# Kernel tuning notes

Hardware: AMD Instinct MI355X
Metric: run time of the kernel (lower is better)

## Reference

```python
import jax, jax.numpy as jnp
import numpy as np

EMB_DIM = 1024
H = 16
HEAD_DIM = EMB_DIM // H
B = 2
S = 2048  # enc and dec seq len
LN_EPS = 1e-5


def setup_inputs() -> dict:
    key = jax.random.key(0)
    ks = jax.random.split(key, 8)
    scale_in = 1.0 / np.sqrt(EMB_DIM)
    scale_o = 1.0 / np.sqrt(H * HEAD_DIM)
    return {
        "enc_out": jax.random.normal(ks[0], (B, S, EMB_DIM), jnp.float32),
        "dec_out": jax.random.normal(ks[1], (B, S, EMB_DIM), jnp.float32),
        # stacked per-head projections, equivalent to h separate Linear(emb_dim, head_dim, bias=False)
        "Wq": jax.random.uniform(ks[2], (H, EMB_DIM, HEAD_DIM), jnp.float32, -scale_in, scale_in),
        "Wk": jax.random.uniform(ks[3], (H, EMB_DIM, HEAD_DIM), jnp.float32, -scale_in, scale_in),
        "Wv": jax.random.uniform(ks[4], (H, EMB_DIM, HEAD_DIM), jnp.float32, -scale_in, scale_in),
        "Wo": jax.random.uniform(ks[5], (H * HEAD_DIM, EMB_DIM), jnp.float32, -scale_o, scale_o),
        "gamma": jnp.ones((EMB_DIM,), jnp.float32),
        "beta": jnp.zeros((EMB_DIM,), jnp.float32),
    }


def reference(enc_out, dec_out, Wq, Wk, Wv, Wo, gamma, beta):
    d = Wq.shape[-1]
    # per-head projections, batched over heads (same math as the Python loop)
    q = jnp.einsum('bse,hed->bhsd', dec_out, Wq)   # queries from decoder
    k = jnp.einsum('bte,hed->bhtd', enc_out, Wk)   # keys from encoder
    v = jnp.einsum('bte,hed->bhtd', enc_out, Wv)   # values from encoder
    scores = jnp.einsum('bhsd,bhtd->bhst', q, k) / jnp.sqrt(jnp.asarray(d, q.dtype))
    att = jax.nn.softmax(scores, axis=-1)
    ctx = jnp.einsum('bhst,bhtd->bhsd', att, v)
    b, h, s, hd = ctx.shape
    ctx = ctx.transpose(0, 2, 1, 3).reshape(b, s, h * hd)  # concat heads along feature dim
    transformed = ctx @ Wo  # dropout is identity in eval mode
    x = dec_out + transformed
    mu = jnp.mean(x, axis=-1, keepdims=True)
    var = jnp.mean(jnp.square(x - mu), axis=-1, keepdims=True)
    return (x - mu) * jax.lax.rsqrt(var + LN_EPS) * gamma + beta
```

## Files before the change

### kernel.cpp

```cpp
#include <hip/hip_runtime.h>
#include <hip/hip_bf16.h>

#define EMB   1024
#define NH    16
#define HD    64
#define SEQ   2048
#define SA    72

typedef __attribute__((ext_vector_type(8))) short          bf16x8;
typedef __attribute__((ext_vector_type(8))) unsigned short us8;
typedef __attribute__((ext_vector_type(4))) float          f32x4;

__device__ __forceinline__ float u2f(unsigned short u) {
    return __uint_as_float(((unsigned)u) << 16);
}
__device__ __forceinline__ unsigned short f2u(float f) {
    __hip_bfloat16 b = __float2bfloat16(f);
    return *reinterpret_cast<unsigned short*>(&b);
}
__device__ __forceinline__ bool detect_bf16(const void* gamma) {
    return ((const unsigned short*)gamma)[0] == 0x3F80;
}
__device__ __forceinline__ f32x4 fzero() {
    f32x4 v; v.x = v.y = v.z = v.w = 0.f; return v;
}
__device__ __forceinline__ void ld16f(const void* p, size_t idx, bool isbf, float* o) {
    if (isbf) {
        const unsigned short* b = (const unsigned short*)p + idx;
        us8 v0 = *(const us8*)b, v1 = *(const us8*)(b + 8);
        #pragma unroll
        for (int i = 0; i < 8; ++i) { o[i] = u2f(v0[i]); o[8 + i] = u2f(v1[i]); }
    } else {
        const float* f = (const float*)p + idx;
        #pragma unroll
        for (int i = 0; i < 4; ++i) {
            float4 v = *(const float4*)(f + 4 * i);
            o[4*i] = v.x; o[4*i+1] = v.y; o[4*i+2] = v.z; o[4*i+3] = v.w;
        }
    }
}
__device__ __forceinline__ float ld1f(const void* p, size_t i, bool isbf) {
    return isbf ? u2f(((const unsigned short*)p)[i]) : ((const float*)p)[i];
}
__device__ __forceinline__ float4 ld4(const void* p, size_t idx, bool isbf) {
    if (isbf) {
        ushort4 t = *reinterpret_cast<const ushort4*>((const unsigned short*)p + idx);
        return make_float4(u2f(t.x), u2f(t.y), u2f(t.z), u2f(t.w));
    }
    return *reinterpret_cast<const float4*>((const float*)p + idx);
}
__device__ __forceinline__ us8 pk8(const float* s) {
    us8 v;
    #pragma unroll
    for (int i = 0; i < 8; ++i) v[i] = f2u(s[i]);
    return v;
}
__device__ __forceinline__ f32x4 mfma16(bf16x8 a, bf16x8 b, f32x4 c) {
    return __builtin_amdgcn_mfma_f32_16x16x32_bf16(a, b, c, 0, 0, 0);
}
__device__ __forceinline__ bf16x8 mk8(unsigned w0, unsigned w1, unsigned w2, unsigned w3) {
    union { unsigned u[4]; bf16x8 v; } x;
    x.u[0] = w0; x.u[1] = w1; x.u[2] = w2; x.u[3] = w3;
    return x.v;
}
__device__ __forceinline__ float fexp2(float x) {
    return __builtin_amdgcn_exp2f(x);
}
__device__ __forceinline__ unsigned cvtpk(float lo, float hi) {
    unsigned r;
    asm("v_cvt_pk_bf16_f32 %0, %1, %2" : "=v"(r) : "v"(lo), "v"(hi));
    return r;
}
__device__ __forceinline__ void gl_lds16(const unsigned short* g, unsigned short* l) {
    __builtin_amdgcn_global_load_lds(
        (const __attribute__((address_space(1))) void*)g,
        (__attribute__((address_space(3))) void*)l,
        16, 0, 0);
}

#define QSCALE 0.18033688f

__global__ __launch_bounds__(256) void prep_kernel(
    const void* __restrict__ dec, const void* __restrict__ enc,
    const void* __restrict__ Wq, const void* __restrict__ Wk,
    const void* __restrict__ Wv, const void* __restrict__ Wo,
    const void* __restrict__ gamma,
    unsigned short* __restrict__ xb,
    unsigned short* __restrict__ wt,
    unsigned short* __restrict__ wot)
{
    const bool isbf = detect_bf16(gamma);
    const int blk = blockIdx.x;
    __shared__ unsigned short T[64][SA];

    if (blk < 2048) {
        const size_t HALF = (size_t)4096 * 1024;
        size_t idx = ((size_t)blk * 256 + threadIdx.x) * 16;
        const void* src; size_t off;
        if (idx < HALF) { src = dec; off = idx; } else { src = enc; off = idx - HALF; }
        float buf[16];
        ld16f(src, off, isbf, buf);
        *(us8*)&xb[idx]     = pk8(buf);
        *(us8*)&xb[idx + 8] = pk8(buf + 8);
    } else if (blk < 2816) {
        const int local = blk - 2048;
        const int which = local >> 8, h = (local >> 4) & 15, e0 = (local & 15) * 64;
        const void* W = (which == 0) ? Wq : (which == 1 ? Wk : Wv);
        const int sr = threadIdx.x >> 2, sc = (threadIdx.x & 3) * 16;

        float buf[16];
        ld16f(W, ((size_t)h * EMB + e0 + sr) * HD + sc, isbf, buf);
        #pragma unroll
        for (int i = 0; i < 16; ++i) T[sc + i][sr] = f2u(buf[i]);
        __syncthreads();
        us8 v0 = *(const us8*)&T[sr][sc];
        us8 v1 = *(const us8*)&T[sr][sc + 8];
        size_t o = (((size_t)which * NH + h) * HD + sr) * EMB + e0 + sc;
        *(us8*)&wt[o] = v0;
        *(us8*)&wt[o + 8] = v1;
    } else {
        const int local = blk - 2816;
        const int n0 = (local & 15) * 64, k0 = (local >> 4) * 64;
        const int sr = threadIdx.x >> 2, sc = (threadIdx.x & 3) * 16;

        float buf[16];
        ld16f(Wo, (size_t)(k0 + sr) * EMB + n0 + sc, isbf, buf);
        #pragma unroll
        for (int i = 0; i < 16; ++i) T[sc + i][sr] = f2u(buf[i]);
        __syncthreads();
        us8 v0 = *(const us8*)&T[sr][sc];
        us8 v1 = *(const us8*)&T[sr][sc + 8];
        size_t o = (size_t)(n0 + sr) * EMB + k0 + sc;
        *(us8*)&wot[o] = v0;
        *(us8*)&wot[o + 8] = v1;
    }
}

__global__ __launch_bounds__(256) void qkv_kernel(
    const unsigned short* __restrict__ xb,
    const unsigned short* __restrict__ wt,
    unsigned short* __restrict__ qo, unsigned short* __restrict__ ko,
    unsigned short* __restrict__ vt)
{
    const int id = blockIdx.x;
    const int xcd = id & 7, sl = id >> 3;
    const int m_t = xcd * 4 + (sl & 3);
    const int n_t = sl >> 2;
    const int m0 = m_t * 128, n0g = n_t * 128;
    const int which = n0g >> 10;
    const int nloc = n0g & 1023;
    const unsigned short* X = xb + ((which == 0) ? (size_t)0 : (size_t)4096 * 1024);

    __shared__ unsigned short smem[17408];
    unsigned short* const ldsA = smem;
    unsigned short* const ldsB = smem + 8192;

    const int tid = threadIdx.x, wv = tid >> 6, lane = tid & 63;
    const int lq = lane >> 4, lm = lane & 15;
    const int mw = (wv & 1) * 64, nw = (wv >> 1) * 64;

    const unsigned short* Wb = wt + (size_t)(which * 1024 + nloc) * EMB;

    const int seg0 = wv * 4;
    const int srow = lane >> 3;
    const int su   = (lane & 7) ^ srow;
    const unsigned short* aP[4];
    const unsigned short* bP[4];
    #pragma unroll
    for (int q = 0; q < 4; ++q) {
        const int s = seg0 + q;
        aP[q] = X  + (size_t)(m0 + 8 * s + srow) * EMB + su * 8;
        bP[q] = Wb + (size_t)(8 * s + srow) * EMB + su * 8;
    }

    f32x4 acc[4][4];
    #pragma unroll
    for (int i = 0; i < 4; ++i)
        #pragma unroll
        for (int j = 0; j < 4; ++j) acc[i][j] = fzero();

    const int xa = lm & 7;

    for (int k0 = 0; k0 < EMB; k0 += 64) {
        #pragma unroll
        for (int q = 0; q < 4; ++q) {
            gl_lds16(aP[q] + k0, ldsA + (seg0 + q) * 512);
            gl_lds16(bP[q] + k0, ldsB + (seg0 + q) * 512);
        }
        asm volatile("s_waitcnt vmcnt(0)" ::: "memory");
        __syncthreads();

        #pragma unroll
        for (int st = 0; st < 2; ++st) {
            const int u = (st * 4 + lq) ^ xa;
            bf16x8 af[4], bq[4];
            #pragma unroll
            for (int i = 0; i < 4; ++i)
                af[i] = *(const bf16x8*)(ldsA + (mw + i * 16 + lm) * 64 + u * 8);
            #pragma unroll
            for (int j = 0; j < 4; ++j)
                bq[j] = *(const bf16x8*)(ldsB + (nw + j * 16 + lm) * 64 + u * 8);
            #pragma unroll
            for (int i = 0; i < 4; ++i)
                #pragma unroll
                for (int j = 0; j < 4; ++j)
                    acc[i][j] = mfma16(af[i], bq[j], acc[i][j]);
        }
        __syncthreads();
    }

    const int b = m0 >> 11, s0 = m0 & (SEQ - 1);
    const float osc = (which == 0) ? QSCALE : 1.0f;
    if (which != 2) {
        unsigned short* Y = which ? ko : qo;
        #pragma unroll
        for (int i = 0; i < 4; ++i)
            #pragma unroll
            for (int j = 0; j < 4; ++j)
                #pragma unroll
                for (int r = 0; r < 4; ++r) {
                    int m = mw + i * 16 + lq * 4 + r;
                    int n = nloc + nw + j * 16 + lm;
                    int h = n >> 6, d = n & 63;
                    Y[(((size_t)b * NH + h) * SEQ + s0 + m) * HD + d] = f2u(acc[i][j][r] * osc);
                }
    } else {
        __syncthreads();
        unsigned short* vbuf = smem;
        #pragma unroll
        for (int i = 0; i < 4; ++i)
            #pragma unroll
            for (int j = 0; j < 4; ++j) {
                ushort4 p;
                p.x = f2u(acc[i][j][0]); p.y = f2u(acc[i][j][1]);
                p.z = f2u(acc[i][j][2]); p.w = f2u(acc[i][j][3]);
                *(ushort4*)&vbuf[(size_t)(nw + j * 16 + lm) * 136 + mw + i * 16 + lq * 4] = p;
            }
        __syncthreads();
        const int dd = tid >> 1, cc = (tid & 1) * 64;
        const int n = nloc + dd, h = n >> 6, d = n & 63;
        size_t o = (((size_t)b * NH + h) * HD + d) * SEQ + s0 + cc;
        #pragma unroll
        for (int jj = 0; jj < 8; ++jj)
            *(us8*)&vt[o + 8 * jj] = *(const us8*)&vbuf[(size_t)dd * 136 + cc + 8 * jj];
    }
}

__global__ __launch_bounds__(128) void attn_kernel(
    const unsigned short* __restrict__ qg,
    const unsigned short* __restrict__ kg,
    const unsigned short* __restrict__ vtg,
    unsigned short* __restrict__ ctx)
{
    __shared__ unsigned short Ks[2][4096];
    __shared__ unsigned short Vt[2][4096];

    const int tid = threadIdx.x, wv = tid >> 6, lane = tid & 63;
    const int lq = lane >> 4, lm = lane & 15;
    const int bh = blockIdx.x, q0 = blockIdx.y * 64;
    const unsigned short* Kg = kg + (size_t)bh * SEQ * HD;
    const unsigned short* Vg = vtg + (size_t)bh * HD * SEQ;

    const int srow = lane >> 3;
    const int su   = (lane & 7) ^ srow;
    const unsigned short* kSp[4];
    const unsigned short* vSp[4];
    #pragma unroll
    for (int j = 0; j < 4; ++j) {
        const int seg = wv + 2 * j;
        kSp[j] = Kg + (size_t)(8 * seg + srow) * HD  + su * 8;
        vSp[j] = Vg + (size_t)(8 * seg + srow) * SEQ + su * 8;
    }

    bf16x8 qf[2][2];
    #pragma unroll
    for (int s = 0; s < 2; ++s)
        #pragma unroll
        for (int st = 0; st < 2; ++st)
            qf[s][st] = *(const bf16x8*)(qg + (size_t)bh * SEQ * HD
                          + (size_t)(q0 + wv * 32 + s * 16 + lm) * HD + st * 32 + lq * 8);

    bf16x8 onesf;
    #pragma unroll
    for (int i = 0; i < 8; ++i) onesf[i] = (short)0x3F80;

    f32x4 Of[2][4], lacc[2];
    #pragma unroll
    for (int s = 0; s < 2; ++s) {
        lacc[s] = fzero();
        #pragma unroll
        for (int t = 0; t < 4; ++t) Of[s][t] = fzero();
    }

    const int xa = lm & 7;

    #pragma unroll
    for (int j = 0; j < 4; ++j) {
        gl_lds16(kSp[j], &Ks[0][(wv + 2 * j) * 512]);
        gl_lds16(vSp[j], &Vt[0][(wv + 2 * j) * 512]);
    }

    for (int it = 0; it < SEQ / 64; ++it) {
        const int cur = it & 1;
        if (it + 1 < SEQ / 64) {
            const size_t ko = (size_t)(it + 1) * 64 * HD;
            const int    vo = (it + 1) * 64;
            #pragma unroll
            for (int j = 0; j < 4; ++j) {
                gl_lds16(kSp[j] + ko, &Ks[cur ^ 1][(wv + 2 * j) * 512]);
                gl_lds16(vSp[j] + vo, &Vt[cur ^ 1][(wv + 2 * j) * 512]);
            }
            asm volatile("s_waitcnt vmcnt(8)" ::: "memory");
        } else {
            asm volatile("s_waitcnt vmcnt(0)" ::: "memory");
        }
        __syncthreads();

        f32x4 sf[2][4];
        #pragma unroll
        for (int s = 0; s < 2; ++s)
            #pragma unroll
            for (int t = 0; t < 4; ++t) sf[s][t] = fzero();
        __builtin_amdgcn_s_setprio(1);
        #pragma unroll
        for (int st = 0; st < 2; ++st) {
            const int u = (st * 4 + lq) ^ xa;
            #pragma unroll
            for (int tt = 0; tt < 4; ++tt) {
                bf16x8 kf = *(const bf16x8*)&Ks[cur][(lm + 16 * tt) * 64 + u * 8];
                sf[0][tt] = mfma16(kf, qf[0][st], sf[0][tt]);
                sf[1][tt] = mfma16(kf, qf[1][st], sf[1][tt]);
            }
        }
        __builtin_amdgcn_s_setprio(0);

        unsigned pw[2][4][2];
        #pragma unroll
        for (int s = 0; s < 2; ++s)
            #pragma unroll
            for (int tt = 0; tt < 4; ++tt) {
                pw[s][tt][0] = cvtpk(fexp2(sf[s][tt][0]), fexp2(sf[s][tt][1]));
                pw[s][tt][1] = cvtpk(fexp2(sf[s][tt][2]), fexp2(sf[s][tt][3]));
            }
        #pragma unroll
        for (int s = 0; s < 2; ++s)
            #pragma unroll
            for (int a = 0; a < 2; ++a)
                #pragma unroll
                for (int c = 0; c < 2; ++c)
                    asm("v_permlane32_swap_b32 %0, %1"
                        : "+v"(pw[s][2 * a][c]), "+v"(pw[s][2 * a + 1][c]));
        #pragma unroll
        for (int s = 0; s < 2; ++s)
            #pragma unroll
            for (int a = 0; a < 2; ++a)
                #pragma unroll
                for (int c = 0; c < 2; ++c)
                    asm("v_permlane16_swap_b32 %0, %1"
                        : "+v"(pw[s][2 * a][c]), "+v"(pw[s][2 * a + 1][c]));

        __builtin_amdgcn_s_setprio(1);
        #pragma unroll
        for (int st = 0; st < 2; ++st) {
            const int u = (st * 4 + lq) ^ xa;
            bf16x8 pf0 = mk8(pw[0][2 * st][0], pw[0][2 * st][1],
                             pw[0][2 * st + 1][0], pw[0][2 * st + 1][1]);
            bf16x8 pf1 = mk8(pw[1][2 * st][0], pw[1][2 * st][1],
                             pw[1][2 * st + 1][0], pw[1][2 * st + 1][1]);
            #pragma unroll
            for (int t = 0; t < 4; ++t) {
                bf16x8 vf = *(const bf16x8*)&Vt[cur][(lm + 16 * t) * 64 + u * 8];
                Of[0][t] = mfma16(pf0, vf, Of[0][t]);
                Of[1][t] = mfma16(pf1, vf, Of[1][t]);
            }
            lacc[0] = mfma16(pf0, onesf, lacc[0]);
            lacc[1] = mfma16(pf1, onesf, lacc[1]);
        }
        __builtin_amdgcn_s_setprio(0);
        __syncthreads();
    }

    const int b = bh >> 4, h = bh & 15;
    #pragma unroll
    for (int s = 0; s < 2; ++s)
        #pragma unroll
        for (int r = 0; r < 4; ++r) {
            float inv = 1.0f / lacc[s][r];
            int srow2 = q0 + wv * 32 + s * 16 + lq * 4 + r;
            #pragma unroll
            for (int t = 0; t < 4; ++t) {
                int d = lm + 16 * t;
                ctx[((size_t)b * SEQ + srow2) * EMB + h * HD + d] = f2u(Of[s][t][r] * inv);
            }
        }
}

__global__ __launch_bounds__(256) void oproj_kernel(
    const unsigned short* __restrict__ ctx,
    const unsigned short* __restrict__ wot,
    const void* __restrict__ dec, const void* __restrict__ gamma,
    float* __restrict__ x)
{
    const bool isbf = detect_bf16(gamma);
    const int id = blockIdx.x;
    const int xcd = id & 7, sl = id >> 3;
    const int m0 = (xcd * 4 + (sl & 3)) * 128;
    const int n0 = (sl >> 2) * 128;

    __shared__ unsigned short smem[16384];
    unsigned short* const ldsA = smem;
    unsigned short* const ldsB = smem + 8192;

    const int tid = threadIdx.x, wv = tid >> 6, lane = tid & 63;
    const int lq = lane >> 4, lm = lane & 15;
    const int mw = (wv & 1) * 64, nw = (wv >> 1) * 64;

    const int seg0 = wv * 4;
    const int srow = lane >> 3;
    const int su   = (lane & 7) ^ srow;
    const unsigned short* aP[4];
    const unsigned short* bP[4];
    #pragma unroll
    for (int q = 0; q < 4; ++q) {
        const int s = seg0 + q;
        aP[q] = ctx + (size_t)(m0 + 8 * s + srow) * EMB + su * 8;
        bP[q] = wot + (size_t)(n0 + 8 * s + srow) * EMB + su * 8;
    }

    f32x4 acc[4][4];
    #pragma unroll
    for (int i = 0; i < 4; ++i)
        #pragma unroll
        for (int j = 0; j < 4; ++j) acc[i][j] = fzero();

    const int xa = lm & 7;

    for (int k0 = 0; k0 < EMB; k0 += 64) {
        #pragma unroll
        for (int q = 0; q < 4; ++q) {
            gl_lds16(aP[q] + k0, ldsA + (seg0 + q) * 512);
            gl_lds16(bP[q] + k0, ldsB + (seg0 + q) * 512);
        }
        asm volatile("s_waitcnt vmcnt(0)" ::: "memory");
        __syncthreads();

        #pragma unroll
        for (int st = 0; st < 2; ++st) {
            const int u = (st * 4 + lq) ^ xa;
            bf16x8 af[4], bq[4];
            #pragma unroll
            for (int i = 0; i < 4; ++i)
                af[i] = *(const bf16x8*)(ldsA + (mw + i * 16 + lm) * 64 + u * 8);
            #pragma unroll
            for (int j = 0; j < 4; ++j)
                bq[j] = *(const bf16x8*)(ldsB + (nw + j * 16 + lm) * 64 + u * 8);
            #pragma unroll
            for (int i = 0; i < 4; ++i)
                #pragma unroll
                for (int j = 0; j < 4; ++j)
                    acc[i][j] = mfma16(af[i], bq[j], acc[i][j]);
        }
        __syncthreads();
    }

    #pragma unroll
    for (int i = 0; i < 4; ++i)
        #pragma unroll
        for (int j = 0; j < 4; ++j)
            #pragma unroll
            for (int r = 0; r < 4; ++r) {
                int m = m0 + mw + i * 16 + lq * 4 + r;
                int n = n0 + nw + j * 16 + lm;
                x[(size_t)m * EMB + n] = acc[i][j][r] + ld1f(dec, (size_t)m * EMB + n, isbf);
            }
}

__global__ __launch_bounds__(256) void ln_kernel(
    const float* __restrict__ x,
    const void* __restrict__ gamma,
    const void* __restrict__ beta,
    void* __restrict__ out)
{
    const bool isbf = detect_bf16(gamma);
    const int row = blockIdx.x;
    const int tid = threadIdx.x;
    const float* xr = x + (size_t)row * EMB;

    float4 xv = *reinterpret_cast<const float4*>(&xr[tid * 4]);
    float s1 = xv.x + xv.y + xv.z + xv.w;
    float s2 = xv.x * xv.x + xv.y * xv.y + xv.z * xv.z + xv.w * xv.w;

    #pragma unroll
    for (int off = 32; off > 0; off >>= 1) {
        s1 += __shfl_down(s1, off);
        s2 += __shfl_down(s2, off);
    }
    __shared__ float w1[4], w2[4];
    const int wid = tid >> 6, lane = tid & 63;
    if (lane == 0) { w1[wid] = s1; w2[wid] = s2; }
    __syncthreads();
    s1 = w1[0] + w1[1] + w1[2] + w1[3];
    s2 = w2[0] + w2[1] + w2[2] + w2[3];

    const float mu  = s1 * (1.0f / EMB);
    const float var = s2 * (1.0f / EMB) - mu * mu;
    const float rs  = rsqrtf(var + 1e-5f);

    float4 gv = ld4(gamma, (size_t)tid * 4, isbf);
    float4 bv = ld4(beta,  (size_t)tid * 4, isbf);
    float4 r;
    r.x = (xv.x - mu) * rs * gv.x + bv.x;
    r.y = (xv.y - mu) * rs * gv.y + bv.y;
    r.z = (xv.z - mu) * rs * gv.z + bv.z;
    r.w = (xv.w - mu) * rs * gv.w + bv.w;

    size_t o = (size_t)row * EMB + tid * 4;
    if (isbf) {
        ushort4 w;
        w.x = f2u(r.x); w.y = f2u(r.y); w.z = f2u(r.z); w.w = f2u(r.w);
        *reinterpret_cast<ushort4*>((unsigned short*)out + o) = w;
    } else {
        *reinterpret_cast<float4*>((float*)out + o) = r;
    }
}

extern "C" void kernel_launch(void* const* d_in, const int* in_sizes, int n_in,
                              void* d_out, int out_size, void* d_ws, size_t ws_size,
                              hipStream_t stream)
{
    const void* enc   = d_in[0];
    const void* dec   = d_in[1];
    const void* Wq    = d_in[2];
    const void* Wk    = d_in[3];
    const void* Wv    = d_in[4];
    const void* Wo    = d_in[5];
    const void* gamma = d_in[6];
    const void* beta  = d_in[7];

    char* w = (char*)d_ws;
    unsigned short* qws  = (unsigned short*)(w);
    unsigned short* kws  = (unsigned short*)(w + (size_t)8  * 1024 * 1024);
    unsigned short* vtws = (unsigned short*)(w + (size_t)16 * 1024 * 1024);
    unsigned short* wtws = (unsigned short*)(w + (size_t)24 * 1024 * 1024);
    unsigned short* wotw = (unsigned short*)(w + (size_t)30 * 1024 * 1024);
    float*          xws  = (float*)         (w);
    unsigned short* xbuf = (unsigned short*)d_out;
    unsigned short* cws  = (unsigned short*)d_out;

    prep_kernel  <<<3072,          256, 0, stream>>>(dec, enc, Wq, Wk, Wv, Wo,
                                                     gamma, xbuf, wtws, wotw);
    qkv_kernel   <<<768,           256, 0, stream>>>(xbuf, wtws, qws, kws, vtws);
    attn_kernel  <<<dim3(32, 32),  128, 0, stream>>>(qws, kws, vtws, cws);
    oproj_kernel <<<256,           256, 0, stream>>>(cws, wotw, dec, gamma, xws);
    ln_kernel    <<<4096,          256, 0, stream>>>(xws, gamma, beta, d_out);
}
```

Before: 239.5 us.

## Split attention KV tile across wave pairs and reduce partial outputs in LDS

The attention block grows from 2 to 4 waves. Each pair of waves handles the same 32 query rows but a different half of each 64-key tile, so per-wave score, exp and PV work is halved. The partial O and row-sum accumulators are combined through shared memory before the final normalization and store. This adds parallelism and latency hiding per block, at the cost of more threads per block, an extra LDS reduction and barrier at the end, and per-wave loads of the full V tile.

```diff
diff --git a/kernel.cpp b/kernel.cpp
--- a/kernel.cpp
+++ b/kernel.cpp
@@ -246,28 +246,29 @@
     }
 }
 
-__global__ __launch_bounds__(128) void attn_kernel(
+__global__ __launch_bounds__(256) void attn_kernel(
     const unsigned short* __restrict__ qg,
     const unsigned short* __restrict__ kg,
     const unsigned short* __restrict__ vtg,
     unsigned short* __restrict__ ctx)
 {
-    __shared__ unsigned short Ks[2][4096];
-    __shared__ unsigned short Vt[2][4096];
+    __shared__ unsigned short smem[16384];
 
     const int tid = threadIdx.x, wv = tid >> 6, lane = tid & 63;
     const int lq = lane >> 4, lm = lane & 15;
+    const int qh  = wv & 1;
+    const int kvh = wv >> 1;
     const int bh = blockIdx.x, q0 = blockIdx.y * 64;
     const unsigned short* Kg = kg + (size_t)bh * SEQ * HD;
     const unsigned short* Vg = vtg + (size_t)bh * HD * SEQ;
 
     const int srow = lane >> 3;
     const int su   = (lane & 7) ^ srow;
-    const unsigned short* kSp[4];
-    const unsigned short* vSp[4];
-    #pragma unroll
-    for (int j = 0; j < 4; ++j) {
-        const int seg = wv + 2 * j;
+    const unsigned short* kSp[2];
+    const unsigned short* vSp[2];
+    #pragma unroll
+    for (int j = 0; j < 2; ++j) {
+        const int seg = wv + 4 * j;
         kSp[j] = Kg + (size_t)(8 * seg + srow) * HD  + su * 8;
         vSp[j] = Vg + (size_t)(8 * seg + srow) * SEQ + su * 8;
     }
@@ -278,7 +279,7 @@
         #pragma unroll
         for (int st = 0; st < 2; ++st)
             qf[s][st] = *(const bf16x8*)(qg + (size_t)bh * SEQ * HD
-                          + (size_t)(q0 + wv * 32 + s * 16 + lm) * HD + st * 32 + lq * 8);
+                          + (size_t)(q0 + qh * 32 + s * 16 + lm) * HD + st * 32 + lq * 8);
 
     bf16x8 onesf;
     #pragma unroll
@@ -293,83 +294,81 @@
     }
 
     const int xa = lm & 7;
-
-    #pragma unroll
-    for (int j = 0; j < 4; ++j) {
-        gl_lds16(kSp[j], &Ks[0][(wv + 2 * j) * 512]);
-        gl_lds16(vSp[j], &Vt[0][(wv + 2 * j) * 512]);
+    const int uv = (kvh * 4 + lq) ^ xa;
+
+    #pragma unroll
+    for (int j = 0; j < 2; ++j) {
+        gl_lds16(kSp[j], smem + (wv + 4 * j) * 512);
+        gl_lds16(vSp[j], smem + 8192 + (wv + 4 * j) * 512);
     }
 
     for (int it = 0; it < SEQ / 64; ++it) {
         const int cur = it & 1;
+        unsigned short* const Kc = smem + cur * 4096;
+        unsigned short* const Vc = smem + 8192 + cur * 4096;
         if (it + 1 < SEQ / 64) {
             const size_t ko = (size_t)(it + 1) * 64 * HD;
             const int    vo = (it + 1) * 64;
-            #pragma unroll
-            for (int j = 0; j < 4; ++j) {
-                gl_lds16(kSp[j] + ko, &Ks[cur ^ 1][(wv + 2 * j) * 512]);
-                gl_lds16(vSp[j] + vo, &Vt[cur ^ 1][(wv + 2 * j) * 512]);
-            }
-            asm volatile("s_waitcnt vmcnt(8)" ::: "memory");
+            unsigned short* const Kn = smem + (cur ^ 1) * 4096;
+            unsigned short* const Vn = smem + 8192 + (cur ^ 1) * 4096;
+            #pragma unroll
+            for (int j = 0; j < 2; ++j) {
+                gl_lds16(kSp[j] + ko, Kn + (wv + 4 * j) * 512);
+                gl_lds16(vSp[j] + vo, Vn + (wv + 4 * j) * 512);
+            }
+            asm volatile("s_waitcnt vmcnt(4)" ::: "memory");
         } else {
             asm volatile("s_waitcnt vmcnt(0)" ::: "memory");
         }
         __syncthreads();
 
-        f32x4 sf[2][4];
+        f32x4 sf[2][2];
         #pragma unroll
         for (int s = 0; s < 2; ++s)
             #pragma unroll
-            for (int t = 0; t < 4; ++t) sf[s][t] = fzero();
+            for (int t = 0; t < 2; ++t) sf[s][t] = fzero();
         __builtin_amdgcn_s_setprio(1);
         #pragma unroll
         for (int st = 0; st < 2; ++st) {
             const int u = (st * 4 + lq) ^ xa;
             #pragma unroll
-            for (int tt = 0; tt < 4; ++tt) {
-                bf16x8 kf = *(const bf16x8*)&Ks[cur][(lm + 16 * tt) * 64 + u * 8];
+            for (int tt = 0; tt < 2; ++tt) {
+                const int ttg = 2 * kvh + tt;
+                bf16x8 kf = *(const bf16x8*)(Kc + (lm + 16 * ttg) * 64 + u * 8);
                 sf[0][tt] = mfma16(kf, qf[0][st], sf[0][tt]);
                 sf[1][tt] = mfma16(kf, qf[1][st], sf[1][tt]);
             }
         }
         __builtin_amdgcn_s_setprio(0);
 
-        unsigned pw[2][4][2];
+        unsigned pw[2][2][2];
         #pragma unroll
         for (int s = 0; s < 2; ++s)
             #pragma unroll
-            for (int tt = 0; tt < 4; ++tt) {
+            for (int tt = 0; tt < 2; ++tt) {
                 pw[s][tt][0] = cvtpk(fexp2(sf[s][tt][0]), fexp2(sf[s][tt][1]));
                 pw[s][tt][1] = cvtpk(fexp2(sf[s][tt][2]), fexp2(sf[s][tt][3]));
             }
         #pragma unroll
         for (int s = 0; s < 2; ++s)
             #pragma unroll
-            for (int a = 0; a < 2; ++a)
-                #pragma unroll
-                for (int c = 0; c < 2; ++c)
-                    asm("v_permlane32_swap_b32 %0, %1"
-                        : "+v"(pw[s][2 * a][c]), "+v"(pw[s][2 * a + 1][c]));
+            for (int c = 0; c < 2; ++c)
+                asm("v_permlane32_swap_b32 %0, %1"
+                    : "+v"(pw[s][0][c]), "+v"(pw[s][1][c]));
         #pragma unroll
         for (int s = 0; s < 2; ++s)
             #pragma unroll
-            for (int a = 0; a < 2; ++a)
-                #pragma unroll
-                for (int c = 0; c < 2; ++c)
-                    asm("v_permlane16_swap_b32 %0, %1"
-                        : "+v"(pw[s][2 * a][c]), "+v"(pw[s][2 * a + 1][c]));
+            for (int c = 0; c < 2; ++c)
+                asm("v_permlane16_swap_b32 %0, %1"
+                    : "+v"(pw[s][0][c]), "+v"(pw[s][1][c]));
 
         __builtin_amdgcn_s_setprio(1);
-        #pragma unroll
-        for (int st = 0; st < 2; ++st) {
-            const int u = (st * 4 + lq) ^ xa;
-            bf16x8 pf0 = mk8(pw[0][2 * st][0], pw[0][2 * st][1],
-                             pw[0][2 * st + 1][0], pw[0][2 * st + 1][1]);
-            bf16x8 pf1 = mk8(pw[1][2 * st][0], pw[1][2 * st][1],
-                             pw[1][2 * st + 1][0], pw[1][2 * st + 1][1]);
+        {
+            bf16x8 pf0 = mk8(pw[0][0][0], pw[0][0][1], pw[0][1][0], pw[0][1][1]);
+            bf16x8 pf1 = mk8(pw[1][0][0], pw[1][0][1], pw[1][1][0], pw[1][1][1]);
             #pragma unroll
             for (int t = 0; t < 4; ++t) {
-                bf16x8 vf = *(const bf16x8*)&Vt[cur][(lm + 16 * t) * 64 + u * 8];
+                bf16x8 vf = *(const bf16x8*)(Vc + (lm + 16 * t) * 64 + uv * 8);
                 Of[0][t] = mfma16(pf0, vf, Of[0][t]);
                 Of[1][t] = mfma16(pf1, vf, Of[1][t]);
             }
@@ -380,19 +379,40 @@
         __syncthreads();
     }
 
-    const int b = bh >> 4, h = bh & 15;
-    #pragma unroll
-    for (int s = 0; s < 2; ++s)
-        #pragma unroll
-        for (int r = 0; r < 4; ++r) {
-            float inv = 1.0f / lacc[s][r];
-            int srow2 = q0 + wv * 32 + s * 16 + lq * 4 + r;
-            #pragma unroll
-            for (int t = 0; t < 4; ++t) {
-                int d = lm + 16 * t;
-                ctx[((size_t)b * SEQ + srow2) * EMB + h * HD + d] = f2u(Of[s][t][r] * inv);
-            }
-        }
+    float* F = (float*)smem;
+    if (kvh == 1) {
+        #pragma unroll
+        for (int s = 0; s < 2; ++s) {
+            #pragma unroll
+            for (int t = 0; t < 4; ++t)
+                *(f32x4*)&F[(((qh * 2 + s) * 4 + t) * 256) + lane * 4] = Of[s][t];
+            *(f32x4*)&F[4096 + (qh * 2 + s) * 256 + lane * 4] = lacc[s];
+        }
+    }
+    __syncthreads();
+    if (kvh == 0) {
+        #pragma unroll
+        for (int s = 0; s < 2; ++s) {
+            #pragma unroll
+            for (int t = 0; t < 4; ++t)
+                Of[s][t] += *(const f32x4*)&F[(((qh * 2 + s) * 4 + t) * 256) + lane * 4];
+            lacc[s] += *(const f32x4*)&F[4096 + (qh * 2 + s) * 256 + lane * 4];
+        }
+
+        const int b = bh >> 4, h = bh & 15;
+        #pragma unroll
+        for (int s = 0; s < 2; ++s)
+            #pragma unroll
+            for (int r = 0; r < 4; ++r) {
+                float inv = 1.0f / lacc[s][r];
+                int srow2 = q0 + qh * 32 + s * 16 + lq * 4 + r;
+                #pragma unroll
+                for (int t = 0; t < 4; ++t) {
+                    int d = lm + 16 * t;
+                    ctx[((size_t)b * SEQ + srow2) * EMB + h * HD + d] = f2u(Of[s][t][r] * inv);
+                }
+            }
+    }
 }
 
 __global__ __launch_bounds__(256) void oproj_kernel(
@@ -550,7 +570,7 @@
     prep_kernel  <<<3072,          256, 0, stream>>>(dec, enc, Wq, Wk, Wv, Wo,
                                                      gamma, xbuf, wtws, wotw);
     qkv_kernel   <<<768,           256, 0, stream>>>(xbuf, wtws, qws, kws, vtws);
-    attn_kernel  <<<dim3(32, 32),  128, 0, stream>>>(qws, kws, vtws, cws);
+    attn_kernel  <<<dim3(32, 32),  256, 0, stream>>>(qws, kws, vtws, cws);
     oproj_kernel <<<256,           256, 0, stream>>>(cws, wotw, dec, gamma, xws);
     ln_kernel    <<<4096,          256, 0, stream>>>(xws, gamma, beta, d_out);
 }
```

Measured after the change: 244.2 us. No clear change (+1.9%).
